# Optimization experiments

Measured on AMD Instinct MI355X. Metric: run time of the kernel, lower is better.

The kernel has to match this reference:

```python
import jax, jax.numpy as jnp
import numpy as np
from jax import lax

V, E, HD, T = 100000, 256, 512, 11
H = HD // 2
B, S = 32, 512
START, STOP = 9, 10
NEG = -10000.0


def _lstm_dir(x, h0, c0, w_ih, w_hh, b_ih, b_hh):
    # x: (time, batch, in). PyTorch gate order i, f, g, o.
    def step(carry, xt):
        h, c = carry
        g = xt @ w_ih.T + b_ih + h @ w_hh.T + b_hh
        i, f, gg, o = jnp.split(g, 4, axis=-1)
        c = jax.nn.sigmoid(f) * c + jax.nn.sigmoid(i) * jnp.tanh(gg)
        h = jax.nn.sigmoid(o) * jnp.tanh(c)
        return (h, c), h
    _, hs = lax.scan(step, (h0, c0), x)
    return hs


def _features(sentence, embed, w_ih_f, w_hh_f, b_ih_f, b_hh_f,
              w_ih_b, w_hh_b, b_ih_b, b_hh_b, h0, c0, w_out, b_out):
    x = embed[sentence]  # (B, S, E)
    # Faithful to original: torch LSTM is seq-first, so it scans over axis 0 (B)
    # with 'batch' dim S (init_hidden uses sentence.shape[1]).
    hf = _lstm_dir(x, h0[0], c0[0], w_ih_f, w_hh_f, b_ih_f, b_hh_f)
    hb = _lstm_dir(x[::-1], h0[1], c0[1], w_ih_b, w_hh_b, b_ih_b, b_hh_b)[::-1]
    out = jnp.concatenate([hf, hb], axis=-1)  # (B, S, HD)
    return out @ w_out.T + b_out  # (B, S, T)


def _viterbi(feats, transitions):
    # feats: (B, S, T); CRF treats dim0 as batch, dim1 as time (as in source).
    delta0 = jnp.full((feats.shape[0], T), NEG, feats.dtype).at[:, START].set(0.0)

    def step(delta, feat_t):
        sc = transitions[None, :, :] + delta[:, None, :]  # (B, T_to, T_from)
        new = sc.max(-1) + feat_t
        return new, jnp.argmax(sc, -1)

    feats_t = jnp.moveaxis(feats[:, 1:], 1, 0)  # (S-1, B, T)
    deltaT, psis = lax.scan(step, delta0, feats_t)
    score = deltaT.max(-1)            # (B,)
    last = jnp.argmax(deltaT, -1)     # (B,)

    def back(nxt, psi_t):
        tag = jnp.take_along_axis(psi_t, nxt[:, None], axis=-1)[:, 0]
        return tag, tag

    _, earlier = lax.scan(back, last, psis, reverse=True)  # (S-1, B)
    path = jnp.concatenate([earlier, last[None, :]], axis=0).T  # (B, S)
    return score, path


def setup_inputs() -> dict:
    key = jax.random.key(0)
    ks = jax.random.split(key, 20)
    sc = 0.05
    sentence = jax.random.randint(ks[0], (B, S), 0, V)
    embed = jax.random.normal(ks[1], (V, E), jnp.float32) * sc
    w_ih_f = jax.random.normal(ks[2], (4 * H, E), jnp.float32) * sc
    w_hh_f = jax.random.normal(ks[3], (4 * H, H), jnp.float32) * sc
    b_ih_f = jax.random.normal(ks[4], (4 * H,), jnp.float32) * sc
    b_hh_f = jax.random.normal(ks[5], (4 * H,), jnp.float32) * sc
    w_ih_b = jax.random.normal(ks[6], (4 * H, E), jnp.float32) * sc
    w_hh_b = jax.random.normal(ks[7], (4 * H, H), jnp.float32) * sc
    b_ih_b = jax.random.normal(ks[8], (4 * H,), jnp.float32) * sc
    b_hh_b = jax.random.normal(ks[9], (4 * H,), jnp.float32) * sc
    h0 = jax.random.normal(ks[10], (2, S, H), jnp.float32)
    c0 = jax.random.normal(ks[11], (2, S, H), jnp.float32)
    w_out = jax.random.normal(ks[12], (T, HD), jnp.float32) * sc
    b_out = jax.random.normal(ks[13], (T,), jnp.float32) * sc
    transitions = jax.random.normal(ks[14], (T, T), jnp.float32)
    transitions = transitions.at[START, :].set(NEG).at[:, STOP].set(NEG)
    return dict(sentence=sentence, embed=embed,
                w_ih_f=w_ih_f, w_hh_f=w_hh_f, b_ih_f=b_ih_f, b_hh_f=b_hh_f,
                w_ih_b=w_ih_b, w_hh_b=w_hh_b, b_ih_b=b_ih_b, b_hh_b=b_hh_b,
                h0=h0, c0=c0, w_out=w_out, b_out=b_out, transitions=transitions)


def reference(sentence, embed, w_ih_f, w_hh_f, b_ih_f, b_hh_f,
              w_ih_b, w_hh_b, b_ih_b, b_hh_b, h0, c0, w_out, b_out, transitions):
    feats = _features(sentence, embed, w_ih_f, w_hh_f, b_ih_f, b_hh_f,
                      w_ih_b, w_hh_b, b_ih_b, b_hh_b, h0, c0, w_out, b_out)
    return _viterbi(feats, transitions)
```

## Files before the change

kernel.cpp:

```cpp
#include <hip/hip_runtime.h>
#include <math.h>


namespace {

constexpr int T_ = 11;
constexpr int HT = 256 * 512;

__device__ __forceinline__ size_t gq_off(int t, int d, int j, int q, int s) {
  return ((((size_t)(t * 2 + d) * 256 + j) * 4 + q) * 512 + s);
}

__global__ __launch_bounds__(256) void k_prep(
    const float* __restrict__ w_ih_f, const float* __restrict__ w_ih_b,
    const float* __restrict__ w_hh_f, const float* __restrict__ w_hh_b,
    const float* __restrict__ b_ih_f, const float* __restrict__ b_hh_f,
    const float* __restrict__ b_ih_b, const float* __restrict__ b_hh_b,
    const float* __restrict__ h0, const float* __restrict__ c0,
    const float* __restrict__ w_out,
    float* __restrict__ wiq, float* __restrict__ wt4, float* __restrict__ bq,
    float* __restrict__ ct, float* __restrict__ ht_f, float* __restrict__ ht_b,
    float* __restrict__ wot) {
  const int i = blockIdx.x * 256 + threadIdx.x;
  if (i < 524288) {
    int d = i >> 18, r = i & 262143, gcr = r >> 8, k = r & 255;
    int q = gcr >> 8, j = gcr & 255;
    const float* w = d ? w_ih_b : w_ih_f;
    wiq[((size_t)(d * 256 + k) * 256 + j) * 4 + q] = w[gcr * 256 + k];
  } else if (i < 1048576) {
    int i2 = i - 524288;
    int d = i2 >> 18, r = i2 & 262143, gcr = r >> 8, k = r & 255;
    int q = gcr >> 8, j = gcr & 255;
    const float* w = d ? w_hh_b : w_hh_f;
    wt4[((size_t)(d * 256 + k) * 256 + j) * 4 + q] = w[gcr * 256 + k];
  } else if (i < 1050624) {
    int r = i - 1048576;
    int d = r >> 10, x = r & 1023, j = x >> 2, q = x & 3;
    const float* bi = d ? b_ih_b : b_ih_f;
    const float* bh = d ? b_hh_b : b_hh_f;
    bq[r] = bi[q * 256 + j] + bh[q * 256 + j];
  } else if (i < 1312768) {
    int r = i - 1050624;
    int d = r >> 17, y = r & 131071, j = y >> 9, s = y & 511;
    ct[r] = c0[((size_t)d * 512 + s) * 256 + j];
  } else if (i < 1574912) {
    int r = i - 1312768;
    int d = r >> 17, y = r & 131071, j = y >> 9, s = y & 511;
    float v = h0[((size_t)d * 512 + s) * 256 + j];
    if (d == 0) ht_f[y] = v; else ht_b[y] = v;
  } else if (i < 1580544) {
    int r = i - 1574912;
    int k = r / 11, tag = r - k * 11;
    wot[r] = w_out[tag * 512 + k];
  }
}

__global__ __launch_bounds__(256) void k_ggemm(
    const int* __restrict__ sent, const float* __restrict__ embed,
    const float* __restrict__ wiq, const float* __restrict__ bq,
    float* __restrict__ Gq) {
  __shared__ float As[64][67];
  const int tid = threadIdx.x;
  const int bid = blockIdx.x;
  const int jg4 = bid & 15;
  const int d = (bid >> 4) & 1;
  const int rt = bid >> 5;
  const int wid = __builtin_amdgcn_readfirstlane(tid >> 6);
  const int lane = tid & 63;
  const int row0 = rt * 64;
  const int t = row0 >> 9;
  const int sb = (row0 & 511) + lane;
  const int j0 = (jg4 * 4 + wid) * 4;

  const int rr = tid & 63, eq = tid >> 6;
  const int tok = sent[row0 + rr];
  const float* erow = embed + (size_t)tok * 256 + eq * 16;

  float acc[16];
#pragma unroll
  for (int g = 0; g < 16; ++g) acc[g] = 0.f;

  const float* wbase = wiq + (size_t)d * 256 * 1024;

  for (int ci = 0; ci < 4; ++ci) {
    const int k0 = ci * 64;
    const float* ep = erow + k0;
    float4 v0 = *(const float4*)(ep);
    float4 v1 = *(const float4*)(ep + 4);
    float4 v2 = *(const float4*)(ep + 8);
    float4 v3 = *(const float4*)(ep + 12);
    const int kb = eq * 16;
    As[kb + 0][rr] = v0.x;  As[kb + 1][rr] = v0.y;  As[kb + 2][rr] = v0.z;  As[kb + 3][rr] = v0.w;
    As[kb + 4][rr] = v1.x;  As[kb + 5][rr] = v1.y;  As[kb + 6][rr] = v1.z;  As[kb + 7][rr] = v1.w;
    As[kb + 8][rr] = v2.x;  As[kb + 9][rr] = v2.y;  As[kb + 10][rr] = v2.z; As[kb + 11][rr] = v2.w;
    As[kb + 12][rr] = v3.x; As[kb + 13][rr] = v3.y; As[kb + 14][rr] = v3.z; As[kb + 15][rr] = v3.w;
    __syncthreads();
#pragma unroll 4
    for (int kk = 0; kk < 64; ++kk) {
      float a = As[kk][lane];
      const float* wp = wbase + (size_t)(k0 + kk) * 1024 + j0 * 4;
#pragma unroll
      for (int g = 0; g < 16; ++g) acc[g] = fmaf(a, wp[g], acc[g]);
    }
    __syncthreads();
  }
  const float* bp = bq + ((size_t)d * 256 + j0) * 4;
#pragma unroll
  for (int g = 0; g < 16; ++g) {
    int jj = g >> 2, q = g & 3;
    Gq[gq_off(t, d, j0 + jj, q, sb)] = acc[g] + bp[g];
  }
}

__global__ __launch_bounds__(512) void k_rstep(
    const float* __restrict__ wt4, const float* __restrict__ Gq,
    float* __restrict__ ht_f, float* __restrict__ ht_b,
    float* __restrict__ ct, int t) {
  __shared__ float red[256][17];
  __shared__ float gb[4][16][65];
  const int tid = threadIdx.x;
  const int bid = blockIdx.x;
  const int jsl = bid & 15, d = (bid >> 4) & 1, sg = bid >> 5;
  const int kh = __builtin_amdgcn_readfirstlane(tid >> 8);
  const int sq = __builtin_amdgcn_readfirstlane((tid >> 6) & 3);
  const int rem = tid & 255;
  const int lane = tid & 63;
  const int j0 = jsl * 16;
  const int s0 = sg * 64 + sq * 16;
  const int tt = d ? 31 - t : t;

  float* htX = d ? ht_b : ht_f;
  const float* hprev = htX + (size_t)t * HT;
  const float* wp = wt4 + ((size_t)d * 256 + (size_t)kh * 128) * 1024 + j0 * 4 + lane;
  const float* hp = hprev + (size_t)kh * 128 * 512 + s0;

  float acc[16];
#pragma unroll
  for (int i = 0; i < 16; ++i) acc[i] = 0.f;

#pragma unroll 4
  for (int k = 0; k < 128; ++k) {
    const float w = wp[(size_t)k * 1024];
    const float* h = hp + (size_t)k * 512;
    float4 h0_ = *(const float4*)(h);
    float4 h1_ = *(const float4*)(h + 4);
    float4 h2_ = *(const float4*)(h + 8);
    float4 h3_ = *(const float4*)(h + 12);
    acc[0]  = fmaf(w, h0_.x, acc[0]);
    acc[1]  = fmaf(w, h0_.y, acc[1]);
    acc[2]  = fmaf(w, h0_.z, acc[2]);
    acc[3]  = fmaf(w, h0_.w, acc[3]);
    acc[4]  = fmaf(w, h1_.x, acc[4]);
    acc[5]  = fmaf(w, h1_.y, acc[5]);
    acc[6]  = fmaf(w, h1_.z, acc[6]);
    acc[7]  = fmaf(w, h1_.w, acc[7]);
    acc[8]  = fmaf(w, h2_.x, acc[8]);
    acc[9]  = fmaf(w, h2_.y, acc[9]);
    acc[10] = fmaf(w, h2_.z, acc[10]);
    acc[11] = fmaf(w, h2_.w, acc[11]);
    acc[12] = fmaf(w, h3_.x, acc[12]);
    acc[13] = fmaf(w, h3_.y, acc[13]);
    acc[14] = fmaf(w, h3_.z, acc[14]);
    acc[15] = fmaf(w, h3_.w, acc[15]);
  }

  if (kh == 1) {
#pragma unroll
    for (int i = 0; i < 16; ++i) red[rem][i] = acc[i];
  }
  __syncthreads();
  if (kh == 0) {
    const int jl = lane >> 2, q = lane & 3;
#pragma unroll
    for (int i = 0; i < 16; ++i) gb[q][jl][sq * 16 + i] = acc[i] + red[rem][i];
  }
  __syncthreads();

  {
    const int jl2 = tid >> 5, sp = tid & 31;
    const int j = j0 + jl2;
    const int sloc = sp * 2;
    const int s = sg * 64 + sloc;
    const float* gp = Gq + gq_off(tt, d, j, 0, s);
    float2 gI = *(const float2*)(gp);
    float2 gF = *(const float2*)(gp + 512);
    float2 gG = *(const float2*)(gp + 1024);
    float2 gO = *(const float2*)(gp + 1536);
    const size_t coff = ((size_t)d * 256 + j) * 512 + s;
    float2 c2 = *(const float2*)(ct + coff);
    float giA[2] = {gI.x, gI.y}, gfA[2] = {gF.x, gF.y};
    float ggA[2] = {gG.x, gG.y}, goA[2] = {gO.x, gO.y};
    float cA[2] = {c2.x, c2.y};
    float cnA[2], hA[2];
#pragma unroll
    for (int e = 0; e < 2; ++e) {
      float gi = gb[0][jl2][sloc + e] + giA[e];
      float gf = gb[1][jl2][sloc + e] + gfA[e];
      float gg = gb[2][jl2][sloc + e] + ggA[e];
      float go = gb[3][jl2][sloc + e] + goA[e];
      float si = 1.f / (1.f + expf(-gi));
      float sf = 1.f / (1.f + expf(-gf));
      float tg = tanhf(gg);
      float so = 1.f / (1.f + expf(-go));
      float cn = sf * cA[e] + si * tg;
      cnA[e] = cn;
      hA[e] = so * tanhf(cn);
    }
    *(float2*)(ct + coff) = make_float2(cnA[0], cnA[1]);
    float* ho = htX + (size_t)(t + 1) * HT + (size_t)j * 512 + s;
    *(float2*)ho = make_float2(hA[0], hA[1]);
  }
}

__global__ __launch_bounds__(256) void k_out(
    const float* __restrict__ ht_f, const float* __restrict__ ht_b,
    const float* __restrict__ wot, const float* __restrict__ b_out,
    float* __restrict__ featsT) {
  __shared__ float red[4][11][64];
  const int tid = threadIdx.x;
  const int bid = blockIdx.x;
  const int t = bid >> 3, stile = bid & 7;
  const int wid = __builtin_amdgcn_readfirstlane(tid >> 6);
  const int lane = tid & 63;
  const int s0 = stile * 64;
  const int kg0 = wid * 128;
  const float* src = (wid < 2)
      ? ht_f + (size_t)(t + 1) * HT + (size_t)kg0 * 512
      : ht_b + (size_t)(32 - t) * HT + (size_t)(kg0 - 256) * 512;

  float acc[11];
#pragma unroll
  for (int g = 0; g < 11; ++g) acc[g] = 0.f;
#pragma unroll 4
  for (int kk = 0; kk < 128; ++kk) {
    float a = src[(size_t)kk * 512 + s0 + lane];
    const float* wp = wot + (size_t)(kg0 + kk) * 11;
#pragma unroll
    for (int g = 0; g < 11; ++g) acc[g] = fmaf(a, wp[g], acc[g]);
  }
#pragma unroll
  for (int g = 0; g < 11; ++g) red[wid][g][lane] = acc[g];
  __syncthreads();
  if (wid == 0) {
#pragma unroll
    for (int g = 0; g < 11; ++g) {
      float v = red[0][g][lane] + red[1][g][lane] + red[2][g][lane] +
                red[3][g][lane] + b_out[g];
      featsT[(size_t)g * 16384 + t * 512 + s0 + lane] = v;
    }
  }
}

#define PAIR(va, ia, vb, ib, vo, io) { bool c_ = (va) >= (vb); vo = c_ ? (va) : (vb); io = c_ ? (ia) : (ib); }

__global__ __launch_bounds__(128) void k_viterbi(const float* __restrict__ featsT,
                                                 const float* __restrict__ trans,
                                                 float* __restrict__ out) {
  __shared__ float fl[512 * T_];
  __shared__ unsigned char psiL[511 * T_];
  __shared__ unsigned char specL[121 * 47];
  __shared__ unsigned char selL[16];
  __shared__ int lastL;
  __shared__ float scoreL;
  const int b = blockIdx.x, tid = threadIdx.x;
  for (int i = tid; i < 512 * T_; i += 128) {
    int tag = i >> 9, s = i & 511;
    fl[s * T_ + tag] = featsT[(size_t)tag * 16384 + b * 512 + s];
  }
  __syncthreads();

  if (tid < 64) {
    const int lane = tid;
    const int to = (lane < T_) ? lane : 0;
    float tr[T_];
#pragma unroll
    for (int f = 0; f < T_; ++f) tr[f] = trans[to * T_ + f];
    float delta = (lane == 9) ? 0.f : -10000.f;

    for (int s = 1; s < 512; ++s) {
      float v0 = tr[0] + __shfl(delta, 0, 64);
      float v1 = tr[1] + __shfl(delta, 1, 64);
      float v2 = tr[2] + __shfl(delta, 2, 64);
      float v3 = tr[3] + __shfl(delta, 3, 64);
      float v4 = tr[4] + __shfl(delta, 4, 64);
      float v5 = tr[5] + __shfl(delta, 5, 64);
      float v6 = tr[6] + __shfl(delta, 6, 64);
      float v7 = tr[7] + __shfl(delta, 7, 64);
      float v8 = tr[8] + __shfl(delta, 8, 64);
      float v9 = tr[9] + __shfl(delta, 9, 64);
      float v10 = tr[10] + __shfl(delta, 10, 64);
      float mA, mB, mC, mD, mE, mG, mH, mI, mJ, m;
      int iA, iB, iC, iD, iE, iG, iH, iI, iJ, am;
      PAIR(v0, 0, v1, 1, mA, iA); PAIR(v2, 2, v3, 3, mB, iB);
      PAIR(v4, 4, v5, 5, mC, iC); PAIR(v6, 6, v7, 7, mD, iD);
      PAIR(v8, 8, v9, 9, mE, iE);
      PAIR(mA, iA, mB, iB, mG, iG); PAIR(mC, iC, mD, iD, mH, iH);
      PAIR(mE, iE, v10, 10, mI, iI);
      PAIR(mG, iG, mH, iH, mJ, iJ);
      PAIR(mJ, iJ, mI, iI, m, am);
      if (lane < T_) psiL[(s - 1) * T_ + lane] = (unsigned char)am;
      delta = m + fl[s * T_ + to];
    }
    float d0 = __shfl(delta, 0, 64), d1 = __shfl(delta, 1, 64);
    float d2 = __shfl(delta, 2, 64), d3 = __shfl(delta, 3, 64);
    float d4 = __shfl(delta, 4, 64), d5 = __shfl(delta, 5, 64);
    float d6 = __shfl(delta, 6, 64), d7 = __shfl(delta, 7, 64);
    float d8 = __shfl(delta, 8, 64), d9 = __shfl(delta, 9, 64);
    float d10 = __shfl(delta, 10, 64);
    float mA, mB, mC, mD, mE, mG, mH, mI, mJ, m;
    int iA, iB, iC, iD, iE, iG, iH, iI, iJ, am;
    PAIR(d0, 0, d1, 1, mA, iA); PAIR(d2, 2, d3, 3, mB, iB);
    PAIR(d4, 4, d5, 5, mC, iC); PAIR(d6, 6, d7, 7, mD, iD);
    PAIR(d8, 8, d9, 9, mE, iE);
    PAIR(mA, iA, mB, iB, mG, iG); PAIR(mC, iC, mD, iD, mH, iH);
    PAIR(mE, iE, d10, 10, mI, iI);
    PAIR(mG, iG, mH, iH, mJ, iJ);
    PAIR(mJ, iJ, mI, iI, m, am);
    if (lane == 0) { lastL = am; scoreL = m; }
  }
  __syncthreads();

  const int last = lastL;
  if (tid < 121) {
    const int g = tid / 11, tau = tid - g * 11;
    const int khi = 510 - 47 * g;
    const int len = (g < 10) ? 47 : 41;
    int cur = tau;
    unsigned char* sp = &specL[(g * 11 + tau) * 47];
    for (int i = 0; i < len; ++i) {
      cur = psiL[(khi - i) * T_ + cur];
      sp[i] = (unsigned char)cur;
    }
  }
  __syncthreads();
  if (tid == 0) {
    int cur = last;
    for (int g = 0; g < 11; ++g) {
      selL[g] = (unsigned char)cur;
      int len = (g < 10) ? 47 : 41;
      cur = specL[(g * 11 + cur) * 47 + (len - 1)];
    }
    out[b] = scoreL;
    out[32 + (size_t)b * 512 + 511] = (float)last;
  }
  __syncthreads();
  if (tid < 121) {
    const int g = tid / 11, tau = tid - g * 11;
    if (tau == selL[g]) {
      const int khi = 510 - 47 * g;
      const int len = (g < 10) ? 47 : 41;
      float* path = out + 32 + (size_t)b * 512;
      const unsigned char* sp = &specL[(g * 11 + tau) * 47];
      for (int i = 0; i < len; ++i) path[khi - i] = (float)sp[i];
    }
  }
}

}

extern "C" void kernel_launch(void* const* d_in, const int* in_sizes, int n_in,
                              void* d_out, int out_size, void* d_ws, size_t ws_size,
                              hipStream_t stream) {
  const int* sent     = (const int*)d_in[0];
  const float* embed  = (const float*)d_in[1];
  const float* w_ih_f = (const float*)d_in[2];
  const float* w_hh_f = (const float*)d_in[3];
  const float* b_ih_f = (const float*)d_in[4];
  const float* b_hh_f = (const float*)d_in[5];
  const float* w_ih_b = (const float*)d_in[6];
  const float* w_hh_b = (const float*)d_in[7];
  const float* b_ih_b = (const float*)d_in[8];
  const float* b_hh_b = (const float*)d_in[9];
  const float* h0     = (const float*)d_in[10];
  const float* c0     = (const float*)d_in[11];
  const float* w_out  = (const float*)d_in[12];
  const float* b_out  = (const float*)d_in[13];
  const float* trans  = (const float*)d_in[14];

  float* ws = (float*)d_ws;
  float* Gq     = ws;
  float* ht_f   = Gq + 33554432;
  float* ht_b   = ht_f + 4325376;
  float* ct     = ht_b + 4325376;
  float* wiq    = ct + 262144;
  float* wt4    = wiq + 524288;
  float* bq     = wt4 + 524288;
  float* wot    = bq + 2048;
  float* featsT = wot + 5632;

  k_prep<<<6174, 256, 0, stream>>>(w_ih_f, w_ih_b, w_hh_f, w_hh_b,
                                   b_ih_f, b_hh_f, b_ih_b, b_hh_b,
                                   h0, c0, w_out,
                                   wiq, wt4, bq, ct, ht_f, ht_b, wot);
  k_ggemm<<<8192, 256, 0, stream>>>(sent, embed, wiq, bq, Gq);
  for (int t = 0; t < 32; ++t)
    k_rstep<<<256, 512, 0, stream>>>(wt4, Gq, ht_f, ht_b, ct, t);
  k_out<<<256, 256, 0, stream>>>(ht_f, ht_b, wot, b_out, featsT);
  k_viterbi<<<32, 128, 0, stream>>>(featsT, trans, (float*)d_out);
}
```

Measured before the change: 816.7 us.

## Retile input GEMM, split recurrent step 4-way over K, simplify Viterbi argmax

The input-projection GEMM now has each thread compute 32 outputs instead of 16 and launches half as many blocks, to get more reuse of each shared-memory A value per weight load. The recurrent step kernel splits the K reduction four ways instead of two and covers 32 sequence positions per block instead of 64, doubling the grid to 512 blocks for better CU occupancy, at the cost of an extra shared-memory reduction. The Viterbi step replaces the paired compare/select argmax tree with an fmax tree plus an equality bitmask and ffs, and loads the emission value earlier to shorten the serial dependency chain. Launch bounds with a minimum of 4 blocks are added, which may limit register use and cause spills for the 32-accumulator GEMM.

```diff
diff --git a/kernel.cpp b/kernel.cpp
--- a/kernel.cpp
+++ b/kernel.cpp
@@ -55,30 +55,30 @@
   }
 }
 
-__global__ __launch_bounds__(256) void k_ggemm(
+__global__ __launch_bounds__(256, 4) void k_ggemm(
     const int* __restrict__ sent, const float* __restrict__ embed,
     const float* __restrict__ wiq, const float* __restrict__ bq,
     float* __restrict__ Gq) {
   __shared__ float As[64][67];
   const int tid = threadIdx.x;
   const int bid = blockIdx.x;
-  const int jg4 = bid & 15;
-  const int d = (bid >> 4) & 1;
-  const int rt = bid >> 5;
+  const int jg8 = bid & 7;
+  const int d = (bid >> 3) & 1;
+  const int rt = bid >> 4;
   const int wid = __builtin_amdgcn_readfirstlane(tid >> 6);
   const int lane = tid & 63;
   const int row0 = rt * 64;
   const int t = row0 >> 9;
   const int sb = (row0 & 511) + lane;
-  const int j0 = (jg4 * 4 + wid) * 4;
+  const int j0 = (jg8 * 4 + wid) * 8;
 
   const int rr = tid & 63, eq = tid >> 6;
   const int tok = sent[row0 + rr];
   const float* erow = embed + (size_t)tok * 256 + eq * 16;
 
-  float acc[16];
-#pragma unroll
-  for (int g = 0; g < 16; ++g) acc[g] = 0.f;
+  float acc[32];
+#pragma unroll
+  for (int g = 0; g < 32; ++g) acc[g] = 0.f;
 
   const float* wbase = wiq + (size_t)d * 256 * 1024;
 
@@ -95,51 +95,51 @@
     As[kb + 8][rr] = v2.x;  As[kb + 9][rr] = v2.y;  As[kb + 10][rr] = v2.z; As[kb + 11][rr] = v2.w;
     As[kb + 12][rr] = v3.x; As[kb + 13][rr] = v3.y; As[kb + 14][rr] = v3.z; As[kb + 15][rr] = v3.w;
     __syncthreads();
-#pragma unroll 4
+#pragma unroll 2
     for (int kk = 0; kk < 64; ++kk) {
       float a = As[kk][lane];
       const float* wp = wbase + (size_t)(k0 + kk) * 1024 + j0 * 4;
 #pragma unroll
-      for (int g = 0; g < 16; ++g) acc[g] = fmaf(a, wp[g], acc[g]);
+      for (int g = 0; g < 32; ++g) acc[g] = fmaf(a, wp[g], acc[g]);
     }
     __syncthreads();
   }
   const float* bp = bq + ((size_t)d * 256 + j0) * 4;
 #pragma unroll
-  for (int g = 0; g < 16; ++g) {
+  for (int g = 0; g < 32; ++g) {
     int jj = g >> 2, q = g & 3;
     Gq[gq_off(t, d, j0 + jj, q, sb)] = acc[g] + bp[g];
   }
 }
 
-__global__ __launch_bounds__(512) void k_rstep(
+__global__ __launch_bounds__(512, 4) void k_rstep(
     const float* __restrict__ wt4, const float* __restrict__ Gq,
     float* __restrict__ ht_f, float* __restrict__ ht_b,
     float* __restrict__ ct, int t) {
-  __shared__ float red[256][17];
-  __shared__ float gb[4][16][65];
+  __shared__ float red[3][128][17];
+  __shared__ float gb[4][16][33];
   const int tid = threadIdx.x;
   const int bid = blockIdx.x;
   const int jsl = bid & 15, d = (bid >> 4) & 1, sg = bid >> 5;
-  const int kh = __builtin_amdgcn_readfirstlane(tid >> 8);
-  const int sq = __builtin_amdgcn_readfirstlane((tid >> 6) & 3);
-  const int rem = tid & 255;
+  const int kh = __builtin_amdgcn_readfirstlane(tid >> 7);
+  const int sq = __builtin_amdgcn_readfirstlane((tid >> 6) & 1);
+  const int rem = tid & 127;
   const int lane = tid & 63;
   const int j0 = jsl * 16;
-  const int s0 = sg * 64 + sq * 16;
+  const int s0 = sg * 32 + sq * 16;
   const int tt = d ? 31 - t : t;
 
   float* htX = d ? ht_b : ht_f;
   const float* hprev = htX + (size_t)t * HT;
-  const float* wp = wt4 + ((size_t)d * 256 + (size_t)kh * 128) * 1024 + j0 * 4 + lane;
-  const float* hp = hprev + (size_t)kh * 128 * 512 + s0;
+  const float* wp = wt4 + ((size_t)d * 256 + (size_t)kh * 64) * 1024 + j0 * 4 + lane;
+  const float* hp = hprev + (size_t)kh * 64 * 512 + s0;
 
   float acc[16];
 #pragma unroll
   for (int i = 0; i < 16; ++i) acc[i] = 0.f;
 
 #pragma unroll 4
-  for (int k = 0; k < 128; ++k) {
+  for (int k = 0; k < 64; ++k) {
     const float w = wp[(size_t)k * 1024];
     const float* h = hp + (size_t)k * 512;
     float4 h0_ = *(const float4*)(h);
@@ -164,51 +164,40 @@
     acc[15] = fmaf(w, h3_.w, acc[15]);
   }
 
-  if (kh == 1) {
-#pragma unroll
-    for (int i = 0; i < 16; ++i) red[rem][i] = acc[i];
+  if (kh > 0) {
+#pragma unroll
+    for (int i = 0; i < 16; ++i) red[kh - 1][rem][i] = acc[i];
   }
   __syncthreads();
   if (kh == 0) {
     const int jl = lane >> 2, q = lane & 3;
 #pragma unroll
-    for (int i = 0; i < 16; ++i) gb[q][jl][sq * 16 + i] = acc[i] + red[rem][i];
+    for (int i = 0; i < 16; ++i) {
+      float v = acc[i] + red[0][rem][i] + red[1][rem][i] + red[2][rem][i];
+      gb[q][jl][sq * 16 + i] = v;
+    }
   }
   __syncthreads();
 
   {
     const int jl2 = tid >> 5, sp = tid & 31;
     const int j = j0 + jl2;
-    const int sloc = sp * 2;
-    const int s = sg * 64 + sloc;
+    const int s = sg * 32 + sp;
     const float* gp = Gq + gq_off(tt, d, j, 0, s);
-    float2 gI = *(const float2*)(gp);
-    float2 gF = *(const float2*)(gp + 512);
-    float2 gG = *(const float2*)(gp + 1024);
-    float2 gO = *(const float2*)(gp + 1536);
+    float gi = gb[0][jl2][sp] + gp[0];
+    float gf = gb[1][jl2][sp] + gp[512];
+    float gg = gb[2][jl2][sp] + gp[1024];
+    float go = gb[3][jl2][sp] + gp[1536];
+    float si = 1.f / (1.f + expf(-gi));
+    float sf = 1.f / (1.f + expf(-gf));
+    float tg = tanhf(gg);
+    float so = 1.f / (1.f + expf(-go));
     const size_t coff = ((size_t)d * 256 + j) * 512 + s;
-    float2 c2 = *(const float2*)(ct + coff);
-    float giA[2] = {gI.x, gI.y}, gfA[2] = {gF.x, gF.y};
-    float ggA[2] = {gG.x, gG.y}, goA[2] = {gO.x, gO.y};
-    float cA[2] = {c2.x, c2.y};
-    float cnA[2], hA[2];
-#pragma unroll
-    for (int e = 0; e < 2; ++e) {
-      float gi = gb[0][jl2][sloc + e] + giA[e];
-      float gf = gb[1][jl2][sloc + e] + gfA[e];
-      float gg = gb[2][jl2][sloc + e] + ggA[e];
-      float go = gb[3][jl2][sloc + e] + goA[e];
-      float si = 1.f / (1.f + expf(-gi));
-      float sf = 1.f / (1.f + expf(-gf));
-      float tg = tanhf(gg);
-      float so = 1.f / (1.f + expf(-go));
-      float cn = sf * cA[e] + si * tg;
-      cnA[e] = cn;
-      hA[e] = so * tanhf(cn);
-    }
-    *(float2*)(ct + coff) = make_float2(cnA[0], cnA[1]);
-    float* ho = htX + (size_t)(t + 1) * HT + (size_t)j * 512 + s;
-    *(float2*)ho = make_float2(hA[0], hA[1]);
+    float cp = ct[coff];
+    float cn = sf * cp + si * tg;
+    float hn = so * tanhf(cn);
+    ct[coff] = cn;
+    htX[(size_t)(t + 1) * HT + (size_t)j * 512 + s] = hn;
   }
 }
 
@@ -251,8 +240,6 @@
   }
 }
 
-#define PAIR(va, ia, vb, ib, vo, io) { bool c_ = (va) >= (vb); vo = c_ ? (va) : (vb); io = c_ ? (ia) : (ib); }
-
 __global__ __launch_bounds__(128) void k_viterbi(const float* __restrict__ featsT,
                                                  const float* __restrict__ trans,
                                                  float* __restrict__ out) {
@@ -278,6 +265,7 @@
     float delta = (lane == 9) ? 0.f : -10000.f;
 
     for (int s = 1; s < 512; ++s) {
+      float fv = fl[s * T_ + to];
       float v0 = tr[0] + __shfl(delta, 0, 64);
       float v1 = tr[1] + __shfl(delta, 1, 64);
       float v2 = tr[2] + __shfl(delta, 2, 64);
@@ -289,17 +277,25 @@
       float v8 = tr[8] + __shfl(delta, 8, 64);
       float v9 = tr[9] + __shfl(delta, 9, 64);
       float v10 = tr[10] + __shfl(delta, 10, 64);
-      float mA, mB, mC, mD, mE, mG, mH, mI, mJ, m;
-      int iA, iB, iC, iD, iE, iG, iH, iI, iJ, am;
-      PAIR(v0, 0, v1, 1, mA, iA); PAIR(v2, 2, v3, 3, mB, iB);
-      PAIR(v4, 4, v5, 5, mC, iC); PAIR(v6, 6, v7, 7, mD, iD);
-      PAIR(v8, 8, v9, 9, mE, iE);
-      PAIR(mA, iA, mB, iB, mG, iG); PAIR(mC, iC, mD, iD, mH, iH);
-      PAIR(mE, iE, v10, 10, mI, iI);
-      PAIR(mG, iG, mH, iH, mJ, iJ);
-      PAIR(mJ, iJ, mI, iI, m, am);
+      float mA = fmaxf(fmaxf(v0, v1), v2);
+      float mB = fmaxf(fmaxf(v3, v4), v5);
+      float mC = fmaxf(fmaxf(v6, v7), v8);
+      float mD = fmaxf(v9, v10);
+      float m = fmaxf(fmaxf(mA, mB), fmaxf(mC, mD));
+      delta = m + fv;
+      unsigned msk = (v0 == m) ? 1u : 0u;
+      msk |= (v1 == m) ? 2u : 0u;
+      msk |= (v2 == m) ? 4u : 0u;
+      msk |= (v3 == m) ? 8u : 0u;
+      msk |= (v4 == m) ? 16u : 0u;
+      msk |= (v5 == m) ? 32u : 0u;
+      msk |= (v6 == m) ? 64u : 0u;
+      msk |= (v7 == m) ? 128u : 0u;
+      msk |= (v8 == m) ? 256u : 0u;
+      msk |= (v9 == m) ? 512u : 0u;
+      msk |= (v10 == m) ? 1024u : 0u;
+      int am = __ffs(msk) - 1;
       if (lane < T_) psiL[(s - 1) * T_ + lane] = (unsigned char)am;
-      delta = m + fl[s * T_ + to];
     }
     float d0 = __shfl(delta, 0, 64), d1 = __shfl(delta, 1, 64);
     float d2 = __shfl(delta, 2, 64), d3 = __shfl(delta, 3, 64);
@@ -307,15 +303,23 @@
     float d6 = __shfl(delta, 6, 64), d7 = __shfl(delta, 7, 64);
     float d8 = __shfl(delta, 8, 64), d9 = __shfl(delta, 9, 64);
     float d10 = __shfl(delta, 10, 64);
-    float mA, mB, mC, mD, mE, mG, mH, mI, mJ, m;
-    int iA, iB, iC, iD, iE, iG, iH, iI, iJ, am;
-    PAIR(d0, 0, d1, 1, mA, iA); PAIR(d2, 2, d3, 3, mB, iB);
-    PAIR(d4, 4, d5, 5, mC, iC); PAIR(d6, 6, d7, 7, mD, iD);
-    PAIR(d8, 8, d9, 9, mE, iE);
-    PAIR(mA, iA, mB, iB, mG, iG); PAIR(mC, iC, mD, iD, mH, iH);
-    PAIR(mE, iE, d10, 10, mI, iI);
-    PAIR(mG, iG, mH, iH, mJ, iJ);
-    PAIR(mJ, iJ, mI, iI, m, am);
+    float mA = fmaxf(fmaxf(d0, d1), d2);
+    float mB = fmaxf(fmaxf(d3, d4), d5);
+    float mC = fmaxf(fmaxf(d6, d7), d8);
+    float mD = fmaxf(d9, d10);
+    float m = fmaxf(fmaxf(mA, mB), fmaxf(mC, mD));
+    unsigned msk = (d0 == m) ? 1u : 0u;
+    msk |= (d1 == m) ? 2u : 0u;
+    msk |= (d2 == m) ? 4u : 0u;
+    msk |= (d3 == m) ? 8u : 0u;
+    msk |= (d4 == m) ? 16u : 0u;
+    msk |= (d5 == m) ? 32u : 0u;
+    msk |= (d6 == m) ? 64u : 0u;
+    msk |= (d7 == m) ? 128u : 0u;
+    msk |= (d8 == m) ? 256u : 0u;
+    msk |= (d9 == m) ? 512u : 0u;
+    msk |= (d10 == m) ? 1024u : 0u;
+    int am = __ffs(msk) - 1;
     if (lane == 0) { lastL = am; scoreL = m; }
   }
   __syncthreads();
@@ -392,9 +396,9 @@
                                    b_ih_f, b_hh_f, b_ih_b, b_hh_b,
                                    h0, c0, w_out,
                                    wiq, wt4, bq, ct, ht_f, ht_b, wot);
-  k_ggemm<<<8192, 256, 0, stream>>>(sent, embed, wiq, bq, Gq);
+  k_ggemm<<<4096, 256, 0, stream>>>(sent, embed, wiq, bq, Gq);
   for (int t = 0; t < 32; ++t)
-    k_rstep<<<256, 512, 0, stream>>>(wt4, Gq, ht_f, ht_b, ct, t);
+    k_rstep<<<512, 512, 0, stream>>>(wt4, Gq, ht_f, ht_b, ct, t);
   k_out<<<256, 256, 0, stream>>>(ht_f, ht_b, wot, b_out, featsT);
   k_viterbi<<<32, 128, 0, stream>>>(featsT, trans, (float*)d_out);
 }
```

Result: faster. 799.8 us (-2.1%).
